# Kernel optimization log

Hardware: AMD Instinct MI355X
Metric: run time of the kernel (lower is better)

The kernel has to match this reference:

```python
import jax, jax.numpy as jnp
import numpy as np

MIN_NORM = 1e-15
BALL_EPS = 1e-5  # projection margin for the Poincare ball


def _tanh(x):
    return jnp.tanh(jnp.clip(x, -15.0, 15.0))


def _artanh(x):
    return jnp.arctanh(jnp.clip(x, -1.0 + 1e-5, 1.0 - 1e-5))


def givens_rotations(r, x):
    # r, x: (N, d) with d even -> (N, d)
    g = r.reshape(r.shape[0], -1, 2)
    g = g / jnp.maximum(jnp.linalg.norm(g, axis=-1, keepdims=True), MIN_NORM)
    xp = x.reshape(x.shape[0], -1, 2)
    swap = jnp.concatenate([-xp[..., 1:], xp[..., :1]], axis=-1)
    return (g[..., :1] * xp + g[..., 1:] * swap).reshape(r.shape[0], -1)


def givens_reflection(r, x):
    g = r.reshape(r.shape[0], -1, 2)
    g = g / jnp.maximum(jnp.linalg.norm(g, axis=-1, keepdims=True), MIN_NORM)
    xp = x.reshape(x.shape[0], -1, 2)
    a = jnp.concatenate([xp[..., :1], -xp[..., 1:]], axis=-1)
    b = jnp.concatenate([xp[..., 1:], xp[..., :1]], axis=-1)
    return (g[..., :1] * a + g[..., 1:] * b).reshape(r.shape[0], -1)


def expmap0(u, c):
    sqrt_c = jnp.sqrt(c)
    u_norm = jnp.maximum(jnp.linalg.norm(u, axis=-1, keepdims=True), MIN_NORM)
    return _tanh(sqrt_c * u_norm) * u / (sqrt_c * u_norm)


def mobius_add(x, y, c):
    x2 = jnp.sum(x * x, -1, keepdims=True)
    y2 = jnp.sum(y * y, -1, keepdims=True)
    xy = jnp.sum(x * y, -1, keepdims=True)
    num = (1 + 2 * c * xy + c * y2) * x + (1 - c * x2) * y
    denom = 1 + 2 * c * xy + c * c * x2 * y2
    return num / jnp.maximum(denom, MIN_NORM)


def project(x, c):
    norm = jnp.maximum(jnp.linalg.norm(x, axis=-1, keepdims=True), MIN_NORM)
    maxnorm = (1.0 - BALL_EPS) / jnp.sqrt(c)
    return jnp.where(norm > maxnorm, x / norm * maxnorm, x)


def hyp_distance_multi_c_bmm(x, v, c):
    # x: (nc, cs, d) queries; v: (nc, ns, d) candidates; c: (nc, cs, 1) curvatures
    sqrt_c = jnp.sqrt(c)                                              # (nc, cs, 1)
    vnorm = jnp.linalg.norm(v, axis=-1, keepdims=True).transpose(0, 2, 1)  # (nc, 1, ns)
    xv = jnp.einsum('bcd,bnd->bcn', x, v) / vnorm                     # (nc, cs, ns)
    gamma = _tanh(sqrt_c * vnorm) / sqrt_c                            # (nc, cs, ns)
    x2 = jnp.sum(x * x, -1, keepdims=True)                            # (nc, cs, 1)
    c1 = 1 - 2 * c * gamma * xv + c * gamma ** 2
    c2 = 1 - c * x2
    num = jnp.sqrt(jnp.maximum(c1 ** 2 * x2 + c2 ** 2 * gamma ** 2 - 2 * c1 * c2 * gamma * xv, 0.0))
    denom = 1 - 2 * c * gamma * xv + c ** 2 * gamma ** 2 * x2
    dist = _artanh(sqrt_c * num / jnp.maximum(denom, MIN_NORM))
    return 2 * dist / sqrt_c                                          # (nc, cs, ns)


def setup_inputs() -> dict:
    key = jax.random.key(0)
    nc, cs, ns, d = 16, 1024, 1024, 512
    B = nc * cs
    ks = jax.random.split(key, 8)
    return {
        'head': jax.random.normal(ks[0], (B, d), jnp.float32),
        'head_bias': jax.random.normal(ks[1], (B, 1), jnp.float32),
        'rel': jax.random.normal(ks[2], (B, d), jnp.float32),
        'rel_diag': jax.random.normal(ks[3], (B, 2 * d), jnp.float32),
        'curvature': jax.random.normal(ks[4], (B, 1), jnp.float32),
        'context': jax.random.normal(ks[5], (B, d), jnp.float32),
        'scale': jnp.full((1,), 1.0 / np.sqrt(d), jnp.float32),
        'tail': jax.random.normal(ks[6], (nc * ns, d), jnp.float32),
        'tail_bias': jax.random.normal(ks[7], (nc * ns, 1), jnp.float32),
        'chunk_size': cs,
        'neg_sample_size': ns,
    }


def reference(head, head_bias, rel, rel_diag, curvature, context, scale, tail,
              tail_bias, chunk_size, neg_sample_size):
    num_chunk = head.shape[0] // chunk_size
    d = head.shape[-1]
    c = jax.nn.softplus(curvature)                                    # (B, 1)
    rot_mat, ref_mat = jnp.split(rel_diag, 2, axis=-1)
    rot_q = givens_rotations(rot_mat, head)[:, None, :]               # (B, 1, d)
    ref_q = givens_reflection(ref_mat, head)[:, None, :]              # (B, 1, d)
    cands = jnp.concatenate([ref_q, rot_q], axis=1)                   # (B, 2, d)
    att_w = jax.nn.softmax(
        jnp.sum(context[:, None, :] * cands * scale, -1, keepdims=True), axis=1)
    att_q = jnp.sum(att_w * cands, axis=1)                            # (B, d)
    lhs = expmap0(att_q, c)
    rel_h = expmap0(rel, c)
    res = project(mobius_add(lhs, rel_h, c), c)                       # (B, d)
    x = res.reshape(num_chunk, chunk_size, d)
    v = tail.reshape(num_chunk, neg_sample_size, d)
    c3 = c.reshape(num_chunk, chunk_size, 1)
    dist = hyp_distance_multi_c_bmm(x, v, c3)                         # (nc, cs, ns)
    score = (-dist ** 2
             + head_bias.reshape(num_chunk, chunk_size, 1)
             + tail_bias.reshape(num_chunk, 1, neg_sample_size))
    return score
```

## Files before the change

### kernel.cpp

```cpp
#include <hip/hip_runtime.h>
#include <math.h>

#define DEV static __device__ __forceinline__

constexpr float MIN_NORM = 1e-15f;
constexpr float BALL_EPS = 1e-5f;
constexpr int D = 512;

typedef float f32x4 __attribute__((ext_vector_type(4)));
typedef short short8v __attribute__((ext_vector_type(8)));
typedef unsigned short ushort8v __attribute__((ext_vector_type(8)));

DEV float wave_sum(float v) {
#pragma unroll
    for (int o = 32; o > 0; o >>= 1) v += __shfl_xor(v, o, 64);
    return v;
}

DEV float tanh_clip(float x) {
    x = fminf(fmaxf(x, -15.0f), 15.0f);
    return tanhf(x);
}

DEV unsigned short f2bf(float f) {
    unsigned int u = __float_as_uint(f);
    u = (u + 0x7FFFu + ((u >> 16) & 1u)) >> 16;
    return (unsigned short)u;
}
DEV float bf2f(unsigned short h) { return __uint_as_float(((unsigned int)h) << 16); }

__global__ __launch_bounds__(64)
void preprocess_kernel(const float* __restrict__ head,
                       const float* __restrict__ rel,
                       const float* __restrict__ rel_diag,
                       const float* __restrict__ curvature,
                       const float* __restrict__ context,
                       const float* __restrict__ scale_p,
                       unsigned short* __restrict__ Ah,
                       unsigned short* __restrict__ Al,
                       float* __restrict__ row_x2,
                       float* __restrict__ row_c,
                       float* __restrict__ row_sc)
{
    const int row  = blockIdx.x;
    const int lane = threadIdx.x;
    const int base = lane * 8;
    const size_t roff = (size_t)row * D;
    const size_t doff = (size_t)row * 2 * D;

    float hv[8], rv[8], gv[8], fv[8], cxv[8];
    *(float4*)&hv[0]  = *(const float4*)(head + roff + base);
    *(float4*)&hv[4]  = *(const float4*)(head + roff + base + 4);
    *(float4*)&rv[0]  = *(const float4*)(rel + roff + base);
    *(float4*)&rv[4]  = *(const float4*)(rel + roff + base + 4);
    *(float4*)&gv[0]  = *(const float4*)(rel_diag + doff + base);
    *(float4*)&gv[4]  = *(const float4*)(rel_diag + doff + base + 4);
    *(float4*)&fv[0]  = *(const float4*)(rel_diag + doff + D + base);
    *(float4*)&fv[4]  = *(const float4*)(rel_diag + doff + D + base + 4);
    *(float4*)&cxv[0] = *(const float4*)(context + roff + base);
    *(float4*)&cxv[4] = *(const float4*)(context + roff + base + 4);

    float rq[8], rf[8];
#pragma unroll
    for (int p = 0; p < 4; ++p) {
        const float x0 = hv[2*p], x1 = hv[2*p+1];
        float g0 = gv[2*p], g1 = gv[2*p+1];
        const float gn = fmaxf(sqrtf(g0*g0 + g1*g1), MIN_NORM);
        g0 /= gn; g1 /= gn;
        rq[2*p]   = g0*x0 - g1*x1;
        rq[2*p+1] = g0*x1 + g1*x0;
        float f0 = fv[2*p], f1 = fv[2*p+1];
        const float fn = fmaxf(sqrtf(f0*f0 + f1*f1), MIN_NORM);
        f0 /= fn; f1 /= fn;
        rf[2*p]   = f0*x0 + f1*x1;
        rf[2*p+1] = f1*x0 - f0*x1;
    }

    float s0=0,s1=0,s2=0,s3=0,s4=0,s5=0,s6=0,s7=0;
#pragma unroll
    for (int e = 0; e < 8; ++e) {
        s0 += cxv[e]*rf[e];   s1 += cxv[e]*rq[e];
        s2 += rv[e]*rv[e];    s3 += rf[e]*rv[e];
        s4 += rq[e]*rv[e];    s5 += rf[e]*rf[e];
        s6 += rq[e]*rq[e];    s7 += rf[e]*rq[e];
    }
    s0 = wave_sum(s0); s1 = wave_sum(s1); s2 = wave_sum(s2); s3 = wave_sum(s3);
    s4 = wave_sum(s4); s5 = wave_sum(s5); s6 = wave_sum(s6); s7 = wave_sum(s7);

    const float cu = curvature[row];
    const float c  = fmaxf(cu, 0.0f) + log1pf(expf(-fabsf(cu)));
    const float sqc = sqrtf(c);
    const float sc  = scale_p[0];

    const float a0 = s0 * sc, a1 = s1 * sc;
    const float mx = fmaxf(a0, a1);
    const float e0 = expf(a0 - mx), e1 = expf(a1 - mx);
    const float w0 = e0 / (e0 + e1);
    const float w1 = 1.0f - w0;

    const float att2    = fmaxf(w0*w0*s5 + 2.0f*w0*w1*s7 + w1*w1*s6, 0.0f);
    const float attdrel = w0*s3 + w1*s4;
    const float u_att = fmaxf(sqrtf(att2), MIN_NORM);
    const float u_rel = fmaxf(sqrtf(s2), MIN_NORM);

    const float kl = tanh_clip(sqc * u_att) / (sqc * u_att);
    const float kr = tanh_clip(sqc * u_rel) / (sqc * u_rel);

    const float x2 = kl*kl*att2;
    const float y2 = kr*kr*s2;
    const float xy = kl*kr*attdrel;

    const float Am  = 1.0f + 2.0f*c*xy + c*y2;
    const float Bm  = 1.0f - c*x2;
    const float den = fmaxf(1.0f + 2.0f*c*xy + c*c*x2*y2, MIN_NORM);
    const float inv_den = 1.0f / den;

    float pre[8];
    float r2p = 0.0f;
#pragma unroll
    for (int e = 0; e < 8; ++e) {
        const float attq = w0*rf[e] + w1*rq[e];
        pre[e] = (Am*kl*attq + Bm*kr*rv[e]) * inv_den;
        r2p += pre[e]*pre[e];
    }
    r2p = wave_sum(r2p);

    const float nrm  = fmaxf(sqrtf(r2p), MIN_NORM);
    const float maxn = (1.0f - BALL_EPS) / sqc;
    const float psc  = (nrm > maxn) ? (maxn / nrm) : 1.0f;

    ushort8v hi, lo;
#pragma unroll
    for (int e = 0; e < 8; ++e) {
        const float o = pre[e] * psc;
        const unsigned short hb_ = f2bf(o);
        hi[e] = hb_;
        lo[e] = f2bf(o - bf2f(hb_));
    }
    *(ushort8v*)(Ah + roff + base) = hi;
    *(ushort8v*)(Al + roff + base) = lo;

    if (lane == 0) {
        row_x2[row] = r2p * psc * psc;
        row_c[row]  = c;
        row_sc[row] = sqc;
    }
}

__global__ __launch_bounds__(64)
void tailprep_kernel(const float* __restrict__ tail,
                     unsigned short* __restrict__ Bh,
                     unsigned short* __restrict__ Bl,
                     float* __restrict__ vnorm)
{
    const int row  = blockIdx.x;
    const int lane = threadIdx.x;
    const size_t roff = (size_t)row * D + lane * 8;
    float v[8];
    *(float4*)&v[0] = *(const float4*)(tail + roff);
    *(float4*)&v[4] = *(const float4*)(tail + roff + 4);
    float s = 0.0f;
    ushort8v hi, lo;
#pragma unroll
    for (int e = 0; e < 8; ++e) {
        s += v[e]*v[e];
        const unsigned short hb_ = f2bf(v[e]);
        hi[e] = hb_;
        lo[e] = f2bf(v[e] - bf2f(hb_));
    }
    s = wave_sum(s);
    *(ushort8v*)(Bh + roff) = hi;
    *(ushort8v*)(Bl + roff) = lo;
    if (lane == 0) vnorm[row] = sqrtf(s);
}

__global__ __launch_bounds__(512, 2)
void score_kernel(const unsigned short* __restrict__ Ah,
                  const unsigned short* __restrict__ Al,
                  const unsigned short* __restrict__ Bh,
                  const unsigned short* __restrict__ Bl,
                  const float* __restrict__ vnorm,
                  const float* __restrict__ row_x2,
                  const float* __restrict__ row_c,
                  const float* __restrict__ row_sc,
                  const float* __restrict__ head_bias,
                  const float* __restrict__ tail_bias,
                  float* __restrict__ out,
                  int cs, int ns)
{
    extern __shared__ __align__(16) char smem[];

    const int bz = blockIdx.z;
    const int m0 = blockIdx.y * 256;
    const int n0 = blockIdx.x * 256;
    const int tid  = threadIdx.x;
    const int lane = tid & 63;
    const int w    = tid >> 6;
    const int wr   = w >> 2, wn = w & 3;
    const int lrow = lane & 15, lg = lane >> 4;

    f32x4 acc[8][4];
#pragma unroll
    for (int i = 0; i < 8; ++i)
#pragma unroll
        for (int j = 0; j < 4; ++j) acc[i][j] = f32x4{0.f, 0.f, 0.f, 0.f};

    const size_t Aoff = (size_t)(bz * cs + m0) * D;
    const size_t Boff = (size_t)(bz * ns + n0) * D;

#define STAGE_PANEL(dstbase, Hi, Lo, Goff, K0)                                     \
    do {                                                                           \
        _Pragma("unroll")                                                          \
        for (int it_ = 0; it_ < 4; ++it_) {                                        \
            const int L_ = it_ * 512 + tid;                                        \
            const int r_ = L_ >> 3, s_ = L_ & 7;                                   \
            const int kc_ = s_ ^ (r_ & 7);                                         \
            const unsigned short* src_ = (kc_ < 4)                                 \
                ? Hi + Goff + (size_t)r_ * D + (K0) + kc_ * 8                      \
                : Lo + Goff + (size_t)r_ * D + (K0) + (kc_ - 4) * 8;               \
            __builtin_amdgcn_global_load_lds(                                      \
                (const __attribute__((address_space(1))) unsigned int*)src_,       \
                (__attribute__((address_space(3))) unsigned int*)((dstbase) + L_ * 16), \
                16, 0, 0);                                                         \
        }                                                                          \
    } while (0)

#define READ_A(M, AH_, AL_)                                                        \
    do {                                                                           \
        const int r_ = wr * 128 + (M) * 16 + lrow;                                 \
        const char* rp_ = curb + r_ * 128;                                         \
        AH_ = *(const short8v*)(rp_ + ((lg    ) ^ (r_ & 7)) * 16);                 \
        AL_ = *(const short8v*)(rp_ + ((lg + 4) ^ (r_ & 7)) * 16);                 \
    } while (0)

#define MFMA_(A_, B_, C_) __builtin_amdgcn_mfma_f32_16x16x32_bf16(A_, B_, C_, 0, 0, 0)

#define TRIPROD(M0, M1)                                                            \
    do {                                                                           \
        _Pragma("unroll") for (int n = 0; n < 4; ++n) acc[M0][n] = MFMA_(ah0, bh[n], acc[M0][n]); \
        _Pragma("unroll") for (int n = 0; n < 4; ++n) acc[M1][n] = MFMA_(ah1, bh[n], acc[M1][n]); \
        _Pragma("unroll") for (int n = 0; n < 4; ++n) acc[M0][n] = MFMA_(ah0, bl[n], acc[M0][n]); \
        _Pragma("unroll") for (int n = 0; n < 4; ++n) acc[M1][n] = MFMA_(ah1, bl[n], acc[M1][n]); \
        _Pragma("unroll") for (int n = 0; n < 4; ++n) acc[M0][n] = MFMA_(al0, bh[n], acc[M0][n]); \
        _Pragma("unroll") for (int n = 0; n < 4; ++n) acc[M1][n] = MFMA_(al1, bh[n], acc[M1][n]); \
    } while (0)

    STAGE_PANEL(smem, Ah, Al, Aoff, 0);
    STAGE_PANEL(smem + 32768, Bh, Bl, Boff, 0);
    __syncthreads();

#pragma unroll 1
    for (int t = 0; t < 16; ++t) {
        char* curb = smem + (t & 1) * 65536;
        char* nxtb = smem + ((t + 1) & 1) * 65536;
        const int k0n = (t + 1) * 32;
        const bool more = (t < 15);

        short8v bh[4], bl[4];
        short8v ah0, al0, ah1, al1;

        if (more) STAGE_PANEL(nxtb, Ah, Al, Aoff, k0n);
#pragma unroll
        for (int n = 0; n < 4; ++n) {
            const int r_ = wn * 64 + n * 16 + lrow;
            const char* rp_ = curb + 32768 + r_ * 128;
            bh[n] = *(const short8v*)(rp_ + ((lg    ) ^ (r_ & 7)) * 16);
            bl[n] = *(const short8v*)(rp_ + ((lg + 4) ^ (r_ & 7)) * 16);
        }
        READ_A(0, ah0, al0);
        READ_A(1, ah1, al1);
        __builtin_amdgcn_s_barrier();
        __builtin_amdgcn_s_setprio(1);
        TRIPROD(0, 1);
        __builtin_amdgcn_s_setprio(0);
        __builtin_amdgcn_s_barrier();

        if (more) STAGE_PANEL(nxtb + 32768, Bh, Bl, Boff, k0n);
        READ_A(2, ah0, al0);
        READ_A(3, ah1, al1);
        __builtin_amdgcn_s_barrier();
        __builtin_amdgcn_s_setprio(1);
        TRIPROD(2, 3);
        __builtin_amdgcn_s_setprio(0);
        __builtin_amdgcn_s_barrier();

        READ_A(4, ah0, al0);
        READ_A(5, ah1, al1);
        __builtin_amdgcn_s_barrier();
        __builtin_amdgcn_s_setprio(1);
        TRIPROD(4, 5);
        __builtin_amdgcn_s_setprio(0);
        __builtin_amdgcn_s_barrier();

        READ_A(6, ah0, al0);
        READ_A(7, ah1, al1);
        __builtin_amdgcn_s_barrier();
        __builtin_amdgcn_s_setprio(1);
        TRIPROD(6, 7);
        __builtin_amdgcn_s_setprio(0);

        __syncthreads();
    }

    const int nbase = n0 + wn * 64 + lrow;
    float rvn[4], vnv[4], tb[4];
#pragma unroll
    for (int j = 0; j < 4; ++j) {
        const int gn = bz * ns + nbase + j * 16;
        const float vn = vnorm[gn];
        vnv[j] = vn;
        rvn[j] = 1.0f / vn;
        tb[j]  = tail_bias[gn];
    }
#pragma unroll
    for (int i = 0; i < 8; ++i) {
#pragma unroll
        for (int q = 0; q < 4; ++q) {
            const int gm = bz * cs + m0 + wr * 128 + i * 16 + lg * 4 + q;
            const float x2  = row_x2[gm];
            const float cc  = row_c[gm];
            const float scq = row_sc[gm];
            const float hb  = head_bias[gm];
            const float rscq = 1.0f / scq;
            float* orow = out + (size_t)gm * ns + nbase;
#pragma unroll
            for (int j = 0; j < 4; ++j) {
                const float xv = acc[i][j][q] * rvn[j];
                float xx = fminf(scq * vnv[j], 15.0f);
                const float ey = __expf(2.0f * xx);
                const float g  = (1.0f - 2.0f / (ey + 1.0f)) * rscq;
                const float c1 = 1.0f - 2.0f*cc*g*xv + cc*g*g;
                const float c2 = 1.0f - cc*x2;
                const float num = sqrtf(fmaxf(c1*c1*x2 + c2*c2*g*g - 2.0f*c1*c2*g*xv, 0.0f));
                const float den = fmaxf(1.0f - 2.0f*cc*g*xv + cc*cc*g*g*x2, MIN_NORM);
                float t = scq * num * __builtin_amdgcn_rcpf(den);
                t = fminf(t, 1.0f - 1e-5f);
                const float ath = 0.5f * __logf((1.0f + t) * __builtin_amdgcn_rcpf(1.0f - t));
                const float dist = 2.0f * rscq * ath;
                orow[j * 16] = -dist * dist + hb + tb[j];
            }
        }
    }
#undef STAGE_PANEL
#undef READ_A
#undef MFMA_
#undef TRIPROD
}

extern "C" void kernel_launch(void* const* d_in, const int* in_sizes, int n_in,
                              void* d_out, int out_size, void* d_ws, size_t ws_size,
                              hipStream_t stream)
{
    const float* head      = (const float*)d_in[0];
    const float* head_bias = (const float*)d_in[1];
    const float* rel       = (const float*)d_in[2];
    const float* rel_diag  = (const float*)d_in[3];
    const float* curvature = (const float*)d_in[4];
    const float* context   = (const float*)d_in[5];
    const float* scale     = (const float*)d_in[6];
    const float* tail      = (const float*)d_in[7];
    const float* tail_bias = (const float*)d_in[8];

    const int B  = in_sizes[1];
    const int T  = in_sizes[8];
    const int ns = out_size / B;
    const int nc = T / ns;
    const int cs = B / nc;

    unsigned short* Ah = (unsigned short*)d_ws;
    unsigned short* Al = Ah + (size_t)B * D;
    unsigned short* Bh = Al + (size_t)B * D;
    unsigned short* Bl = Bh + (size_t)T * D;
    float* row_x2 = (float*)(Bl + (size_t)T * D);
    float* row_c  = row_x2 + B;
    float* row_sc = row_c + B;
    float* vnormb = row_sc + B;

    preprocess_kernel<<<B, 64, 0, stream>>>(head, rel, rel_diag, curvature, context,
                                            scale, Ah, Al, row_x2, row_c, row_sc);
    tailprep_kernel<<<T, 64, 0, stream>>>(tail, Bh, Bl, vnormb);

    (void)hipFuncSetAttribute((const void*)score_kernel,
                              hipFuncAttributeMaxDynamicSharedMemorySize, 131072);
    dim3 grid(ns / 256, cs / 256, nc);
    score_kernel<<<grid, 512, 131072, stream>>>(Ah, Al, Bh, Bl, vnormb, row_x2, row_c,
                                                row_sc, head_bias, tail_bias,
                                                (float*)d_out, cs, ns);
}
```

Measured before the change: 145.7 us.

## Pre-pack bf16 hi/lo operands into swizzled K-block layout and remap workgroups

The preprocessing kernels now write the hi/lo bf16 split of each row into a K-blocked, pre-swizzled packed layout, so each 32-wide K panel of a 256-row tile is one contiguous 32KB region. The score kernel can then stage panels with plain linear global_load_lds copies, with no per-lane address computation or hi/lo selection. The prefetch is split into four half-panel chunks spread across the four compute phases. The grid is flattened with a hardcoded XCD-style block remap that assumes 4x4 tiles per chunk and 256 blocks. This remap is tied to specific problem dimensions and may break or mis-map blocks for other shapes.

```diff
diff --git a/kernel.cpp b/kernel.cpp
--- a/kernel.cpp
+++ b/kernel.cpp
@@ -28,6 +28,17 @@
     return (unsigned short)u;
 }
 DEV float bf2f(unsigned short h) { return __uint_as_float(((unsigned int)h) << 16); }
+
+DEV void write_packed_row(unsigned short* pack, size_t nrow, int row,
+                          int lane, ushort8v hi, ushort8v lo)
+{
+    const int kb  = lane >> 2;
+    const int cch = lane & 3;
+    const int rx  = row & 7;
+    unsigned short* dst = pack + ((size_t)kb * nrow + row) * 64;
+    *(ushort8v*)(dst + ((cch ^ rx) * 8))       = hi;
+    *(ushort8v*)(dst + (((cch + 4) ^ rx) * 8)) = lo;
+}
 
 __global__ __launch_bounds__(64)
 void preprocess_kernel(const float* __restrict__ head,
@@ -36,11 +47,11 @@
                        const float* __restrict__ curvature,
                        const float* __restrict__ context,
                        const float* __restrict__ scale_p,
-                       unsigned short* __restrict__ Ah,
-                       unsigned short* __restrict__ Al,
+                       unsigned short* __restrict__ packA,
                        float* __restrict__ row_x2,
                        float* __restrict__ row_c,
-                       float* __restrict__ row_sc)
+                       float* __restrict__ row_sc,
+                       int nrow)
 {
     const int row  = blockIdx.x;
     const int lane = threadIdx.x;
@@ -137,8 +148,7 @@
         hi[e] = hb_;
         lo[e] = f2bf(o - bf2f(hb_));
     }
-    *(ushort8v*)(Ah + roff + base) = hi;
-    *(ushort8v*)(Al + roff + base) = lo;
+    write_packed_row(packA, (size_t)nrow, row, lane, hi, lo);
 
     if (lane == 0) {
         row_x2[row] = r2p * psc * psc;
@@ -149,9 +159,9 @@
 
 __global__ __launch_bounds__(64)
 void tailprep_kernel(const float* __restrict__ tail,
-                     unsigned short* __restrict__ Bh,
-                     unsigned short* __restrict__ Bl,
-                     float* __restrict__ vnorm)
+                     unsigned short* __restrict__ packB,
+                     float* __restrict__ vnorm,
+                     int nrow)
 {
     const int row  = blockIdx.x;
     const int lane = threadIdx.x;
@@ -169,16 +179,13 @@
         lo[e] = f2bf(v[e] - bf2f(hb_));
     }
     s = wave_sum(s);
-    *(ushort8v*)(Bh + roff) = hi;
-    *(ushort8v*)(Bl + roff) = lo;
+    write_packed_row(packB, (size_t)nrow, row, lane, hi, lo);
     if (lane == 0) vnorm[row] = sqrtf(s);
 }
 
 __global__ __launch_bounds__(512, 2)
-void score_kernel(const unsigned short* __restrict__ Ah,
-                  const unsigned short* __restrict__ Al,
-                  const unsigned short* __restrict__ Bh,
-                  const unsigned short* __restrict__ Bl,
+void score_kernel(const unsigned short* __restrict__ packA,
+                  const unsigned short* __restrict__ packB,
                   const float* __restrict__ vnorm,
                   const float* __restrict__ row_x2,
                   const float* __restrict__ row_c,
@@ -186,13 +193,18 @@
                   const float* __restrict__ head_bias,
                   const float* __restrict__ tail_bias,
                   float* __restrict__ out,
-                  int cs, int ns)
+                  int cs, int ns, int nrowA, int nrowB)
 {
     extern __shared__ __align__(16) char smem[];
 
-    const int bz = blockIdx.z;
-    const int m0 = blockIdx.y * 256;
-    const int n0 = blockIdx.x * 256;
+    const int orig = blockIdx.x;
+    const int wg = (orig & 7) * 32 + (orig >> 3);
+    const int bz = wg >> 4;
+    const int by = (wg >> 2) & 3;
+    const int bx = wg & 3;
+    const int m0 = by * 256;
+    const int n0 = bx * 256;
+
     const int tid  = threadIdx.x;
     const int lane = tid & 63;
     const int w    = tid >> 6;
@@ -205,24 +217,22 @@
 #pragma unroll
         for (int j = 0; j < 4; ++j) acc[i][j] = f32x4{0.f, 0.f, 0.f, 0.f};
 
-    const size_t Aoff = (size_t)(bz * cs + m0) * D;
-    const size_t Boff = (size_t)(bz * ns + n0) * D;
-
-#define STAGE_PANEL(dstbase, Hi, Lo, Goff, K0)                                     \
+    const char* srcA0 = (const char*)packA + (size_t)(bz * cs + m0) * 128;
+    const char* srcB0 = (const char*)packB + (size_t)(bz * ns + n0) * 128;
+    const size_t strideA = (size_t)nrowA * 128;
+    const size_t strideB = (size_t)nrowB * 128;
+
+#define STAGE_HALF(dst, src, half)                                                 \
     do {                                                                           \
-        _Pragma("unroll")                                                          \
-        for (int it_ = 0; it_ < 4; ++it_) {                                        \
-            const int L_ = it_ * 512 + tid;                                        \
-            const int r_ = L_ >> 3, s_ = L_ & 7;                                   \
-            const int kc_ = s_ ^ (r_ & 7);                                         \
-            const unsigned short* src_ = (kc_ < 4)                                 \
-                ? Hi + Goff + (size_t)r_ * D + (K0) + kc_ * 8                      \
-                : Lo + Goff + (size_t)r_ * D + (K0) + (kc_ - 4) * 8;               \
-            __builtin_amdgcn_global_load_lds(                                      \
-                (const __attribute__((address_space(1))) unsigned int*)src_,       \
-                (__attribute__((address_space(3))) unsigned int*)((dstbase) + L_ * 16), \
-                16, 0, 0);                                                         \
-        }                                                                          \
+        const int bo_ = (half) * 16384 + tid * 16;                                 \
+        __builtin_amdgcn_global_load_lds(                                          \
+            (const __attribute__((address_space(1))) unsigned int*)((src) + bo_),  \
+            (__attribute__((address_space(3))) unsigned int*)((dst) + bo_),        \
+            16, 0, 0);                                                             \
+        __builtin_amdgcn_global_load_lds(                                          \
+            (const __attribute__((address_space(1))) unsigned int*)((src) + bo_ + 8192), \
+            (__attribute__((address_space(3))) unsigned int*)((dst) + bo_ + 8192), \
+            16, 0, 0);                                                             \
     } while (0)
 
 #define READ_A(M, AH_, AL_)                                                        \
@@ -245,21 +255,24 @@
         _Pragma("unroll") for (int n = 0; n < 4; ++n) acc[M1][n] = MFMA_(al1, bh[n], acc[M1][n]); \
     } while (0)
 
-    STAGE_PANEL(smem, Ah, Al, Aoff, 0);
-    STAGE_PANEL(smem + 32768, Bh, Bl, Boff, 0);
+    STAGE_HALF(smem,         srcA0, 0);
+    STAGE_HALF(smem,         srcA0, 1);
+    STAGE_HALF(smem + 32768, srcB0, 0);
+    STAGE_HALF(smem + 32768, srcB0, 1);
     __syncthreads();
 
 #pragma unroll 1
     for (int t = 0; t < 16; ++t) {
         char* curb = smem + (t & 1) * 65536;
         char* nxtb = smem + ((t + 1) & 1) * 65536;
-        const int k0n = (t + 1) * 32;
+        const char* srcA_n = srcA0 + (size_t)(t + 1) * strideA;
+        const char* srcB_n = srcB0 + (size_t)(t + 1) * strideB;
         const bool more = (t < 15);
 
         short8v bh[4], bl[4];
         short8v ah0, al0, ah1, al1;
 
-        if (more) STAGE_PANEL(nxtb, Ah, Al, Aoff, k0n);
+        if (more) STAGE_HALF(nxtb + 32768, srcB_n, 0);
 #pragma unroll
         for (int n = 0; n < 4; ++n) {
             const int r_ = wn * 64 + n * 16 + lrow;
@@ -275,7 +288,7 @@
         __builtin_amdgcn_s_setprio(0);
         __builtin_amdgcn_s_barrier();
 
-        if (more) STAGE_PANEL(nxtb + 32768, Bh, Bl, Boff, k0n);
+        if (more) STAGE_HALF(nxtb + 32768, srcB_n, 1);
         READ_A(2, ah0, al0);
         READ_A(3, ah1, al1);
         __builtin_amdgcn_s_barrier();
@@ -284,6 +297,7 @@
         __builtin_amdgcn_s_setprio(0);
         __builtin_amdgcn_s_barrier();
 
+        if (more) STAGE_HALF(nxtb, srcA_n, 0);
         READ_A(4, ah0, al0);
         READ_A(5, ah1, al1);
         __builtin_amdgcn_s_barrier();
@@ -292,6 +306,7 @@
         __builtin_amdgcn_s_setprio(0);
         __builtin_amdgcn_s_barrier();
 
+        if (more) STAGE_HALF(nxtb, srcA_n, 1);
         READ_A(6, ah0, al0);
         READ_A(7, ah1, al1);
         __builtin_amdgcn_s_barrier();
@@ -341,7 +356,7 @@
             }
         }
     }
-#undef STAGE_PANEL
+#undef STAGE_HALF
 #undef READ_A
 #undef MFMA_
 #undef TRIPROD
@@ -367,23 +382,21 @@
     const int nc = T / ns;
     const int cs = B / nc;
 
-    unsigned short* Ah = (unsigned short*)d_ws;
-    unsigned short* Al = Ah + (size_t)B * D;
-    unsigned short* Bh = Al + (size_t)B * D;
-    unsigned short* Bl = Bh + (size_t)T * D;
-    float* row_x2 = (float*)(Bl + (size_t)T * D);
+    unsigned short* packA = (unsigned short*)d_ws;
+    unsigned short* packB = packA + (size_t)16 * B * 64;
+    float* row_x2 = (float*)(packB + (size_t)16 * T * 64);
     float* row_c  = row_x2 + B;
     float* row_sc = row_c + B;
     float* vnormb = row_sc + B;
 
     preprocess_kernel<<<B, 64, 0, stream>>>(head, rel, rel_diag, curvature, context,
-                                            scale, Ah, Al, row_x2, row_c, row_sc);
-    tailprep_kernel<<<T, 64, 0, stream>>>(tail, Bh, Bl, vnormb);
+                                            scale, packA, row_x2, row_c, row_sc, B);
+    tailprep_kernel<<<T, 64, 0, stream>>>(tail, packB, vnormb, T);
 
     (void)hipFuncSetAttribute((const void*)score_kernel,
                               hipFuncAttributeMaxDynamicSharedMemorySize, 131072);
-    dim3 grid(ns / 256, cs / 256, nc);
-    score_kernel<<<grid, 512, 131072, stream>>>(Ah, Al, Bh, Bl, vnormb, row_x2, row_c,
+    const int nblk = (ns / 256) * (cs / 256) * nc;
+    score_kernel<<<nblk, 512, 131072, stream>>>(packA, packB, vnormb, row_x2, row_c,
                                                 row_sc, head_bias, tail_bias,
-                                                (float*)d_out, cs, ns);
-}
+                                                (float*)d_out, cs, ns, B, T);
+}
```

Measured after the change: 136.8 us. -6.2%, faster.
